# Performance work log

Hardware: AMD Instinct MI355X
Metric: run time of the kernel (lower is better)

The kernel has to match this reference:

```python
import jax, jax.numpy as jnp
import numpy as np

K = 64          # number of instance ids (0 = background, skipped)
MARGIN = 1.0    # TripletMarginLoss margin
EPS = 1e-6      # torch pairwise_distance eps (added to the difference)
NCAND = 16      # random negative candidates per instance


def setup_inputs() -> dict:
    key = jax.random.key(0)
    k1, k2 = jax.random.split(key)
    sem_logits = jax.random.normal(k1, (4, 19, 1024, 1024), dtype=jnp.float32)
    instance_mask = jax.random.randint(k2, (1024, 1024), 0, K, dtype=jnp.int32)
    return {"sem_logits": sem_logits, "instance_mask": instance_mask}


def reference(sem_logits, instance_mask):
    B, C, H, W = sem_logits.shape
    HW = H * W
    sem_flat = sem_logits.reshape(B * C, HW)           # [BC, HW]
    mask_flat = instance_mask.reshape(HW)
    ar = jnp.arange(HW, dtype=jnp.int32)

    # first and second pixel (row-major order) of each instance id, vectorized
    first = jax.ops.segment_min(ar, mask_flat, num_segments=K)   # int32 max if empty
    ar2 = jnp.where(ar == first[mask_flat], jnp.int32(HW), ar)
    second = jax.ops.segment_min(ar2, mask_flat, num_segments=K)
    counts = jax.ops.segment_sum(jnp.ones_like(ar), mask_flat, num_segments=K)

    ids = jnp.arange(K, dtype=jnp.int32)
    valid = (counts >= 2) & (ids != 0)

    # random negative: first candidate pixel whose instance id differs
    cand = jax.random.randint(jax.random.key(1), (K, NCAND), 0, HW, dtype=jnp.int32)
    cand_ok = mask_flat[cand] != ids[:, None]
    pick = jnp.argmax(cand_ok, axis=1)
    neg = cand[jnp.arange(K), pick]

    f = jnp.clip(first, 0, HW - 1)
    s = jnp.clip(second, 0, HW - 1)

    a = sem_flat[:, f].T    # [K, B*C] anchor vectors (flattened per-pixel logits)
    p = sem_flat[:, s].T    # positive
    n = sem_flat[:, neg].T  # negative

    d_ap = jnp.linalg.norm(a - p + EPS, axis=1)
    d_an = jnp.linalg.norm(a - n + EPS, axis=1)
    per_inst = jnp.maximum(d_ap - d_an + MARGIN, 0.0)

    cnt = jnp.sum(valid)
    total = jnp.sum(jnp.where(valid, per_inst, 0.0))
    return jnp.where(cnt > 0, total / cnt, jnp.float32(0.0))
```

## Files before the change

### kernel.cpp

```cpp
#include <hip/hip_runtime.h>
#include <stdint.h>

#define HW        (1024 * 1024)
#define KIDS      64
#define NCANDS    16
#define BCC       76
#define EPSF      1e-6f
#define MARGINF   1.0f
#define SENTINEL  0x7FFFFFFF

#define JAX_PARTITIONABLE 1

__device__ __forceinline__ uint32_t rotl32(uint32_t v, int r) {
    return (v << r) | (v >> (32 - r));
}

__device__ void threefry2x32(uint32_t k0, uint32_t k1, uint32_t x0, uint32_t x1,
                             uint32_t* o0, uint32_t* o1) {
    const uint32_t ks2 = k0 ^ k1 ^ 0x1BD11BDAu;
    const int R0[4] = {13, 15, 26, 6};
    const int R1[4] = {17, 29, 16, 24};
    x0 += k0; x1 += k1;
#pragma unroll
    for (int i = 0; i < 4; i++) { x0 += x1; x1 = rotl32(x1, R0[i]); x1 ^= x0; }
    x0 += k1; x1 += ks2 + 1u;
#pragma unroll
    for (int i = 0; i < 4; i++) { x0 += x1; x1 = rotl32(x1, R1[i]); x1 ^= x0; }
    x0 += ks2; x1 += k0 + 2u;
#pragma unroll
    for (int i = 0; i < 4; i++) { x0 += x1; x1 = rotl32(x1, R0[i]); x1 ^= x0; }
    x0 += k0; x1 += k1 + 3u;
#pragma unroll
    for (int i = 0; i < 4; i++) { x0 += x1; x1 = rotl32(x1, R1[i]); x1 ^= x0; }
    x0 += k1; x1 += ks2 + 4u;
#pragma unroll
    for (int i = 0; i < 4; i++) { x0 += x1; x1 = rotl32(x1, R0[i]); x1 ^= x0; }
    x0 += ks2; x1 += k0 + 5u;
    *o0 = x0; *o1 = x1;
}

__device__ uint32_t jax_cand_bits(uint32_t j) {
#if JAX_PARTITIONABLE
    uint32_t k2a, k2b;
    threefry2x32(0u, 1u, 0u, 1u, &k2a, &k2b);
    uint32_t b1, b2;
    threefry2x32(k2a, k2b, 0u, j, &b1, &b2);
    return b1 ^ b2;
#else
    uint32_t a0, a1, b0, b1;
    threefry2x32(0u, 1u, 0u, 2u, &a0, &a1);
    threefry2x32(0u, 1u, 1u, 3u, &b0, &b1);
    uint32_t k2a = a1, k2b = b1;
    uint32_t r0, r1;
    if (j < 512u) { threefry2x32(k2a, k2b, j, j + 512u, &r0, &r1); return r0; }
    else          { threefry2x32(k2a, k2b, j - 512u, j, &r0, &r1); return r1; }
#endif
}

__global__ void k_init(int* g_first, int* g_second, int* g_count,
                       float* g_total, int* g_cnt) {
    int t = threadIdx.x;
    if (t < KIDS) { g_first[t] = SENTINEL; g_second[t] = SENTINEL; g_count[t] = 0; }
    if (t == 0)   { *g_total = 0.0f; *g_cnt = 0; }
}

__global__ void k_seg(const int* __restrict__ mask,
                      int* g_first, int* g_second, int* g_count) {
    __shared__ int m1[KIDS], m2[KIDS], cnt[KIDS];
    const int t = threadIdx.x;
    if (t < KIDS) { m1[t] = SENTINEL; m2[t] = SENTINEL; cnt[t] = 0; }
    __syncthreads();

    const int4* m4 = (const int4*)mask;
    const int base4 = blockIdx.x * 1024;
    int4 v[4];
#pragma unroll
    for (int c = 0; c < 4; c++) v[c] = m4[base4 + c * 256 + t];

#pragma unroll
    for (int c = 0; c < 4; c++) {
        const int pix0 = (base4 + c * 256 + t) * 4;
        const int ids[4] = {v[c].x, v[c].y, v[c].z, v[c].w};
#pragma unroll
        for (int j = 0; j < 4; j++) {
            atomicAdd(&cnt[ids[j]], 1);
            atomicMin(&m1[ids[j]], pix0 + j);
        }
    }
    __syncthreads();
#pragma unroll
    for (int c = 0; c < 4; c++) {
        const int pix0 = (base4 + c * 256 + t) * 4;
        const int ids[4] = {v[c].x, v[c].y, v[c].z, v[c].w};
#pragma unroll
        for (int j = 0; j < 4; j++) {
            if (pix0 + j != m1[ids[j]]) atomicMin(&m2[ids[j]], pix0 + j);
        }
    }
    __syncthreads();

    if (t < KIDS && cnt[t] > 0) {
        const int lm1 = m1[t];
        const int old = atomicMin(&g_first[t], lm1);
        const int disp = old > lm1 ? old : lm1;
        if (disp != SENTINEL)  atomicMin(&g_second[t], disp);
        if (m2[t] != SENTINEL) atomicMin(&g_second[t], m2[t]);
        atomicAdd(&g_count[t], cnt[t]);
    }
}

__global__ void k_triplet(const float* __restrict__ sem,
                          const int* __restrict__ mask,
                          const int* __restrict__ g_first,
                          const int* __restrict__ g_second,
                          const int* __restrict__ g_count,
                          float* g_total, int* g_cnt) {
    const int k = blockIdx.x;
    if (k == 0 || g_count[k] < 2) return;

    __shared__ int s_neg;
    __shared__ float red_ap[128], red_an[128];
    const int t = threadIdx.x;

    if (t == 0) {
        int neg = -1, first_cand = -1;
        for (int c = 0; c < NCANDS; c++) {
            const uint32_t bits = jax_cand_bits((uint32_t)(k * NCANDS + c));
            const int cand = (int)(bits & (uint32_t)(HW - 1));
            if (c == 0) first_cand = cand;
            if (neg < 0 && mask[cand] != k) neg = cand;
        }
        s_neg = (neg < 0) ? first_cand : neg;
    }
    __syncthreads();

    const int f = g_first[k], s = g_second[k], n = s_neg;
    float ap = 0.0f, an = 0.0f;
    if (t < BCC) {
        const size_t row = (size_t)t * (size_t)HW;
        const float a  = sem[row + f];
        const float p  = sem[row + s];
        const float nn = sem[row + n];
        const float d1 = a - p + EPSF;
        const float d2 = a - nn + EPSF;
        ap = d1 * d1;
        an = d2 * d2;
    }
    red_ap[t] = ap; red_an[t] = an;
    __syncthreads();
    for (int off = 64; off > 0; off >>= 1) {
        if (t < off) { red_ap[t] += red_ap[t + off]; red_an[t] += red_an[t + off]; }
        __syncthreads();
    }
    if (t == 0) {
        float per = sqrtf(red_ap[0]) - sqrtf(red_an[0]) + MARGINF;
        per = per > 0.0f ? per : 0.0f;
        atomicAdd(g_total, per);
        atomicAdd(g_cnt, 1);
    }
}

__global__ void k_final(const float* __restrict__ g_total,
                        const int* __restrict__ g_cnt, float* out) {
    const int c = *g_cnt;
    out[0] = (c > 0) ? (*g_total / (float)c) : 0.0f;
}

extern "C" void kernel_launch(void* const* d_in, const int* in_sizes, int n_in,
                              void* d_out, int out_size, void* d_ws, size_t ws_size,
                              hipStream_t stream) {
    const float* sem  = (const float*)d_in[0];
    const int*   mask = (const int*)d_in[1];
    float* out = (float*)d_out;

    int* ws = (int*)d_ws;
    int* g_first  = ws;
    int* g_second = ws + 64;
    int* g_count  = ws + 128;
    float* g_total = (float*)(ws + 192);
    int*   g_cnt   = ws + 193;

    k_init<<<1, 64, 0, stream>>>(g_first, g_second, g_count, g_total, g_cnt);
    k_seg<<<HW / 4096, 256, 0, stream>>>(mask, g_first, g_second, g_count);
    k_triplet<<<KIDS, 128, 0, stream>>>(sem, mask, g_first, g_second, g_count,
                                        g_total, g_cnt);
    k_final<<<1, 1, 0, stream>>>(g_total, g_cnt, out);
}
```

Baseline: 360.3 us.

## Single-pass segment min tracking, parallel negative pick, fuse final reduction

The segment kernel now finds first and second pixel per id in one atomic pass, using the displaced value from atomicMin, and drops the count array and second barrier pass. The per-instance negative search hashes the 16 candidates in parallel across lanes and picks one with a ballot, replacing a serial loop on thread 0. The constant split key is computed at compile time with constexpr threefry. The final-division kernel is replaced by a last-block-done counter inside the triplet kernel, removing one launch at the cost of a threadfence and extra atomics.

```diff
diff --git a/kernel.cpp b/kernel.cpp
--- a/kernel.cpp
+++ b/kernel.cpp
@@ -7,163 +7,141 @@
 #define BCC       76
 #define EPSF      1e-6f
 #define MARGINF   1.0f
-#define SENTINEL  0x7FFFFFFF
+#define SENT      0xFFFFFFFFu
 
-#define JAX_PARTITIONABLE 1
-
-__device__ __forceinline__ uint32_t rotl32(uint32_t v, int r) {
+__host__ __device__ constexpr uint32_t rotl32c(uint32_t v, int r) {
     return (v << r) | (v >> (32 - r));
 }
 
-__device__ void threefry2x32(uint32_t k0, uint32_t k1, uint32_t x0, uint32_t x1,
-                             uint32_t* o0, uint32_t* o1) {
+__host__ __device__ constexpr uint64_t tf2x32(uint32_t k0, uint32_t k1,
+                                              uint32_t x0, uint32_t x1) {
     const uint32_t ks2 = k0 ^ k1 ^ 0x1BD11BDAu;
     const int R0[4] = {13, 15, 26, 6};
     const int R1[4] = {17, 29, 16, 24};
     x0 += k0; x1 += k1;
-#pragma unroll
-    for (int i = 0; i < 4; i++) { x0 += x1; x1 = rotl32(x1, R0[i]); x1 ^= x0; }
+    for (int i = 0; i < 4; i++) { x0 += x1; x1 = rotl32c(x1, R0[i]); x1 ^= x0; }
     x0 += k1; x1 += ks2 + 1u;
-#pragma unroll
-    for (int i = 0; i < 4; i++) { x0 += x1; x1 = rotl32(x1, R1[i]); x1 ^= x0; }
+    for (int i = 0; i < 4; i++) { x0 += x1; x1 = rotl32c(x1, R1[i]); x1 ^= x0; }
     x0 += ks2; x1 += k0 + 2u;
-#pragma unroll
-    for (int i = 0; i < 4; i++) { x0 += x1; x1 = rotl32(x1, R0[i]); x1 ^= x0; }
+    for (int i = 0; i < 4; i++) { x0 += x1; x1 = rotl32c(x1, R0[i]); x1 ^= x0; }
     x0 += k0; x1 += k1 + 3u;
-#pragma unroll
-    for (int i = 0; i < 4; i++) { x0 += x1; x1 = rotl32(x1, R1[i]); x1 ^= x0; }
+    for (int i = 0; i < 4; i++) { x0 += x1; x1 = rotl32c(x1, R1[i]); x1 ^= x0; }
     x0 += k1; x1 += ks2 + 4u;
-#pragma unroll
-    for (int i = 0; i < 4; i++) { x0 += x1; x1 = rotl32(x1, R0[i]); x1 ^= x0; }
+    for (int i = 0; i < 4; i++) { x0 += x1; x1 = rotl32c(x1, R0[i]); x1 ^= x0; }
     x0 += ks2; x1 += k0 + 5u;
-    *o0 = x0; *o1 = x1;
+    return ((uint64_t)x0 << 32) | x1;
 }
 
-__device__ uint32_t jax_cand_bits(uint32_t j) {
-#if JAX_PARTITIONABLE
-    uint32_t k2a, k2b;
-    threefry2x32(0u, 1u, 0u, 1u, &k2a, &k2b);
-    uint32_t b1, b2;
-    threefry2x32(k2a, k2b, 0u, j, &b1, &b2);
-    return b1 ^ b2;
-#else
-    uint32_t a0, a1, b0, b1;
-    threefry2x32(0u, 1u, 0u, 2u, &a0, &a1);
-    threefry2x32(0u, 1u, 1u, 3u, &b0, &b1);
-    uint32_t k2a = a1, k2b = b1;
-    uint32_t r0, r1;
-    if (j < 512u) { threefry2x32(k2a, k2b, j, j + 512u, &r0, &r1); return r0; }
-    else          { threefry2x32(k2a, k2b, j - 512u, j, &r0, &r1); return r1; }
-#endif
+constexpr uint64_t SPLIT1 = tf2x32(0u, 1u, 0u, 1u);
+constexpr uint32_t K2A = (uint32_t)(SPLIT1 >> 32);
+constexpr uint32_t K2B = (uint32_t)SPLIT1;
+
+__device__ __forceinline__ uint32_t jax_cand_bits(uint32_t j) {
+    const uint64_t r = tf2x32(K2A, K2B, 0u, j);
+    return (uint32_t)(r >> 32) ^ (uint32_t)r;
 }
 
-__global__ void k_init(int* g_first, int* g_second, int* g_count,
-                       float* g_total, int* g_cnt) {
-    int t = threadIdx.x;
-    if (t < KIDS) { g_first[t] = SENTINEL; g_second[t] = SENTINEL; g_count[t] = 0; }
-    if (t == 0)   { *g_total = 0.0f; *g_cnt = 0; }
+__global__ void k_init(uint32_t* g_first, uint32_t* g_second,
+                       float* g_total, int* g_cnt, int* g_done) {
+    const int t = threadIdx.x;
+    if (t < KIDS) { g_first[t] = SENT; g_second[t] = SENT; }
+    if (t == 0)   { *g_total = 0.0f; *g_cnt = 0; *g_done = 0; }
 }
 
-__global__ void k_seg(const int* __restrict__ mask,
-                      int* g_first, int* g_second, int* g_count) {
-    __shared__ int m1[KIDS], m2[KIDS], cnt[KIDS];
+__global__ __launch_bounds__(256) void
+k_seg(const int* __restrict__ mask, uint32_t* g_first, uint32_t* g_second) {
+    __shared__ uint32_t m1[KIDS], m2[KIDS];
     const int t = threadIdx.x;
-    if (t < KIDS) { m1[t] = SENTINEL; m2[t] = SENTINEL; cnt[t] = 0; }
+    if (t < KIDS) { m1[t] = SENT; m2[t] = SENT; }
     __syncthreads();
 
     const int4* m4 = (const int4*)mask;
     const int base4 = blockIdx.x * 1024;
-    int4 v[4];
-#pragma unroll
-    for (int c = 0; c < 4; c++) v[c] = m4[base4 + c * 256 + t];
-
 #pragma unroll
     for (int c = 0; c < 4; c++) {
-        const int pix0 = (base4 + c * 256 + t) * 4;
-        const int ids[4] = {v[c].x, v[c].y, v[c].z, v[c].w};
+        const int4 v = m4[base4 + c * 256 + t];
+        const uint32_t pix0 = (uint32_t)(base4 + c * 256 + t) * 4u;
+        const int ids[4] = {v.x, v.y, v.z, v.w};
 #pragma unroll
         for (int j = 0; j < 4; j++) {
-            atomicAdd(&cnt[ids[j]], 1);
-            atomicMin(&m1[ids[j]], pix0 + j);
-        }
-    }
-    __syncthreads();
-#pragma unroll
-    for (int c = 0; c < 4; c++) {
-        const int pix0 = (base4 + c * 256 + t) * 4;
-        const int ids[4] = {v[c].x, v[c].y, v[c].z, v[c].w};
-#pragma unroll
-        for (int j = 0; j < 4; j++) {
-            if (pix0 + j != m1[ids[j]]) atomicMin(&m2[ids[j]], pix0 + j);
+            const uint32_t pix = pix0 + j;
+            const uint32_t old = atomicMin(&m1[ids[j]], pix);
+            const uint32_t disp = old > pix ? old : pix;
+            if (disp != SENT) atomicMin(&m2[ids[j]], disp);
         }
     }
     __syncthreads();
 
-    if (t < KIDS && cnt[t] > 0) {
-        const int lm1 = m1[t];
-        const int old = atomicMin(&g_first[t], lm1);
-        const int disp = old > lm1 ? old : lm1;
-        if (disp != SENTINEL)  atomicMin(&g_second[t], disp);
-        if (m2[t] != SENTINEL) atomicMin(&g_second[t], m2[t]);
-        atomicAdd(&g_count[t], cnt[t]);
+    if (t < KIDS && m1[t] != SENT) {
+        const uint32_t lm1 = m1[t];
+        const uint32_t old = atomicMin(&g_first[t], lm1);
+        const uint32_t disp = old > lm1 ? old : lm1;
+        if (disp != SENT)  atomicMin(&g_second[t], disp);
+        if (m2[t] != SENT) atomicMin(&g_second[t], m2[t]);
     }
 }
 
-__global__ void k_triplet(const float* __restrict__ sem,
-                          const int* __restrict__ mask,
-                          const int* __restrict__ g_first,
-                          const int* __restrict__ g_second,
-                          const int* __restrict__ g_count,
-                          float* g_total, int* g_cnt) {
+__global__ __launch_bounds__(128) void
+k_triplet(const float* __restrict__ sem, const int* __restrict__ mask,
+          const uint32_t* __restrict__ g_first,
+          const uint32_t* __restrict__ g_second,
+          float* g_total, int* g_cnt, int* g_done, float* out) {
     const int k = blockIdx.x;
-    if (k == 0 || g_count[k] < 2) return;
+    const int t = threadIdx.x;
+    const uint32_t f = g_first[k], s = g_second[k];
+    const bool valid = (k != 0) && (s < (uint32_t)HW);
 
     __shared__ int s_neg;
     __shared__ float red_ap[128], red_an[128];
-    const int t = threadIdx.x;
 
+    if (valid) {
+        if (t < 64) {
+            uint32_t cand = 0; bool ok = false;
+            if (t < NCANDS) {
+                cand = jax_cand_bits((uint32_t)(k * NCANDS + t)) & (HW - 1);
+                ok = (mask[cand] != k);
+            }
+            const unsigned long long bal = __ballot(ok);
+            const int pick = bal ? (__ffsll(bal) - 1) : 0;
+            const int neg = __shfl((int)cand, pick);
+            if (t == 0) s_neg = neg;
+        }
+        __syncthreads();
+
+        const int n = s_neg;
+        float ap = 0.0f, an = 0.0f;
+        if (t < BCC) {
+            const size_t row = (size_t)t * (size_t)HW;
+            const float a  = sem[row + f];
+            const float p  = sem[row + s];
+            const float nn = sem[row + n];
+            const float d1 = a - p + EPSF;
+            const float d2 = a - nn + EPSF;
+            ap = d1 * d1; an = d2 * d2;
+        }
+        red_ap[t] = ap; red_an[t] = an;
+        __syncthreads();
+        for (int off = 64; off > 0; off >>= 1) {
+            if (t < off) { red_ap[t] += red_ap[t + off]; red_an[t] += red_an[t + off]; }
+            __syncthreads();
+        }
+        if (t == 0) {
+            float per = sqrtf(red_ap[0]) - sqrtf(red_an[0]) + MARGINF;
+            per = per > 0.0f ? per : 0.0f;
+            atomicAdd(g_total, per);
+            atomicAdd(g_cnt, 1);
+        }
+    }
+
+    __threadfence();
     if (t == 0) {
-        int neg = -1, first_cand = -1;
-        for (int c = 0; c < NCANDS; c++) {
-            const uint32_t bits = jax_cand_bits((uint32_t)(k * NCANDS + c));
-            const int cand = (int)(bits & (uint32_t)(HW - 1));
-            if (c == 0) first_cand = cand;
-            if (neg < 0 && mask[cand] != k) neg = cand;
+        const int done = atomicAdd(g_done, 1);
+        if (done == KIDS - 1) {
+            const float total = atomicAdd(g_total, 0.0f);
+            const int   cnt   = atomicAdd(g_cnt, 0);
+            out[0] = (cnt > 0) ? (total / (float)cnt) : 0.0f;
         }
-        s_neg = (neg < 0) ? first_cand : neg;
     }
-    __syncthreads();
-
-    const int f = g_first[k], s = g_second[k], n = s_neg;
-    float ap = 0.0f, an = 0.0f;
-    if (t < BCC) {
-        const size_t row = (size_t)t * (size_t)HW;
-        const float a  = sem[row + f];
-        const float p  = sem[row + s];
-        const float nn = sem[row + n];
-        const float d1 = a - p + EPSF;
-        const float d2 = a - nn + EPSF;
-        ap = d1 * d1;
-        an = d2 * d2;
-    }
-    red_ap[t] = ap; red_an[t] = an;
-    __syncthreads();
-    for (int off = 64; off > 0; off >>= 1) {
-        if (t < off) { red_ap[t] += red_ap[t + off]; red_an[t] += red_an[t + off]; }
-        __syncthreads();
-    }
-    if (t == 0) {
-        float per = sqrtf(red_ap[0]) - sqrtf(red_an[0]) + MARGINF;
-        per = per > 0.0f ? per : 0.0f;
-        atomicAdd(g_total, per);
-        atomicAdd(g_cnt, 1);
-    }
-}
-
-__global__ void k_final(const float* __restrict__ g_total,
-                        const int* __restrict__ g_cnt, float* out) {
-    const int c = *g_cnt;
-    out[0] = (c > 0) ? (*g_total / (float)c) : 0.0f;
 }
 
 extern "C" void kernel_launch(void* const* d_in, const int* in_sizes, int n_in,
@@ -173,16 +151,15 @@
     const int*   mask = (const int*)d_in[1];
     float* out = (float*)d_out;
 
-    int* ws = (int*)d_ws;
-    int* g_first  = ws;
-    int* g_second = ws + 64;
-    int* g_count  = ws + 128;
-    float* g_total = (float*)(ws + 192);
-    int*   g_cnt   = ws + 193;
+    uint32_t* ws = (uint32_t*)d_ws;
+    uint32_t* g_first  = ws;
+    uint32_t* g_second = ws + 64;
+    float*    g_total  = (float*)(ws + 128);
+    int*      g_cnt    = (int*)(ws + 129);
+    int*      g_done   = (int*)(ws + 130);
 
-    k_init<<<1, 64, 0, stream>>>(g_first, g_second, g_count, g_total, g_cnt);
-    k_seg<<<HW / 4096, 256, 0, stream>>>(mask, g_first, g_second, g_count);
-    k_triplet<<<KIDS, 128, 0, stream>>>(sem, mask, g_first, g_second, g_count,
-                                        g_total, g_cnt);
-    k_final<<<1, 1, 0, stream>>>(g_total, g_cnt, out);
+    k_init<<<1, 64, 0, stream>>>(g_first, g_second, g_total, g_cnt, g_done);
+    k_seg<<<HW / 4096, 256, 0, stream>>>(mask, g_first, g_second);
+    k_triplet<<<KIDS, 128, 0, stream>>>(sem, mask, g_first, g_second,
+                                        g_total, g_cnt, g_done, out);
 }
```

Measured after the change: 361.5 us. Within noise of the previous version (+0.3%).
